# Performance work log

Hardware: AMD Instinct MI355X
Metric: run time of the kernel (lower is better)

Reference implementation:

```python
import jax, jax.numpy as jnp
import numpy as np

NEG_SLOPE = 0.01  # torch LeakyReLU default
MIN_FREQ = 1.0
MAX_FREQ = 10.0
W = 100
N_HIDDEN = 100
N_OBS = 64

def _leaky(x):
    return jnp.where(x >= 0, x, NEG_SLOPE * x)

def setup_inputs() -> dict:
    key = jax.random.key(0)
    ks = jax.random.split(key, 7)
    # kaiming_uniform-ish init scales (exact init doesn't matter for correctness baseline)
    def unif(k, shape, fan_in):
        bound = np.sqrt(6.0 / fan_in)
        return jax.random.uniform(k, shape, jnp.float32, -bound, bound)
    x = jax.random.normal(ks[0], (65536, N_OBS), jnp.float32)
    W_in = unif(ks[1], (N_OBS, W), N_OBS)
    b_in = jnp.zeros((W,), jnp.float32)
    Ws = unif(ks[2], (N_HIDDEN, W, W), W)
    bs = jnp.zeros((N_HIDDEN, W), jnp.float32)
    W_out = unif(ks[3], (W, 1), W)
    b_out = jnp.zeros((1,), jnp.float32)
    return {"x": x, "W_in": W_in, "b_in": b_in, "Ws": Ws, "bs": bs,
            "W_out": W_out, "b_out": b_out}

def reference(x, W_in, b_in, Ws, bs, W_out, b_out):
    h = _leaky(x @ W_in + b_in)                       # [B, 100]
    def layer(h, wb):
        w, b = wb
        return _leaky(h @ w + b), None
    h, _ = jax.lax.scan(layer, h, (Ws, bs))           # 100 hidden layers
    a = h @ W_out + b_out                             # [B, 1]
    a = jnp.tanh(a)
    return (a + 1.0) / 2.0 * (MAX_FREQ - MIN_FREQ) + MIN_FREQ
```

## Files before the change

kernel.cpp:

```cpp
#include <hip/hip_runtime.h>
#include <cmath>

#define NLAYERS 100
#define DIN     64
#define WDIM    100
#define NTT     4
#define ROWS    32
#define KS      7
#define PSTR    136
#define BUF     (ROWS * PSTR)

typedef _Float16 half8  __attribute__((ext_vector_type(8)));
typedef _Float16 half2v __attribute__((ext_vector_type(2)));
typedef __fp16   fp16x2 __attribute__((ext_vector_type(2)));
typedef float    f32x4  __attribute__((ext_vector_type(4)));
typedef float    f32x16 __attribute__((ext_vector_type(16)));

#define WSH_LAYER_HALVES (KS * NTT * 64 * 8)
#define WSH_HALVES       (NLAYERS * WSH_LAYER_HALVES)
#define W0_HALVES        (4 * NTT * 64 * 8)
#define BPAD_FLOATS      128
#define OFF_BPAD_B       ((WSH_HALVES + W0_HALVES) * 2)
#define OFF_WOUT_B       (OFF_BPAD_B + BPAD_FLOATS * 4)
#define WOUT_FLOATS      128

__global__ __launch_bounds__(256)
void actor_prep(const float* __restrict__ Win, const float* __restrict__ bin,
                const float* __restrict__ Ws,  const float* __restrict__ bs,
                const float* __restrict__ Wout,
                _Float16* __restrict__ wsh, _Float16* __restrict__ w0sh,
                float* __restrict__ bpad, float* __restrict__ woutp) {
    __shared__ float tile[16 * 128];
    const int bid = blockIdx.x, tid = threadIdx.x;
    if (bid < NLAYERS * KS) {
        const int l = bid / KS, ks = bid % KS;
#pragma unroll
        for (int e = 0; e < 8; ++e) {
            int idx = tid + 256 * e;
            int kk = idx >> 7, nn = idx & 127;
            int k = ks * 16 + kk;
            float v = 0.f;
            if (k < WDIM && nn < WDIM)        v = Ws[(l * WDIM + k) * WDIM + nn];
            else if (k == WDIM && nn < WDIM)  v = bs[l * WDIM + nn];
            else if (k == WDIM && nn == WDIM) v = 1.0f;
            tile[idx] = v;
        }
        __syncthreads();
        const int lane = tid & 63, nt = tid >> 6;
        const int g = lane >> 5, n = nt * 32 + (lane & 31);
        half8 o;
#pragma unroll
        for (int j = 0; j < 8; ++j) o[j] = (_Float16)tile[(g * 8 + j) * 128 + n];
        *(half8*)(wsh + (((l * KS + ks) * NTT + nt) << 9) + lane * 8) = o;
        return;
    }
    int b2 = bid - NLAYERS * KS;
    if (b2 < 4) {
        const int ks = b2;
#pragma unroll
        for (int e = 0; e < 8; ++e) {
            int idx = tid + 256 * e;
            int kk = idx >> 7, nn = idx & 127;
            int k = ks * 16 + kk;
            tile[idx] = (nn < WDIM) ? Win[k * WDIM + nn] : 0.f;
        }
        __syncthreads();
        const int lane = tid & 63, nt = tid >> 6;
        const int g = lane >> 5, n = nt * 32 + (lane & 31);
        half8 o;
#pragma unroll
        for (int j = 0; j < 8; ++j) o[j] = (_Float16)tile[(g * 8 + j) * 128 + n];
        *(half8*)(w0sh + ((ks * NTT + nt) << 9) + lane * 8) = o;
        return;
    }
    if (tid < BPAD_FLOATS) {
        bpad[tid] = (tid < WDIM) ? bin[tid] : (tid == WDIM ? 1.0f : 0.f);
    } else {
        int t = tid - BPAD_FLOATS;
        if (t < WOUT_FLOATS) woutp[t] = (t < WDIM) ? Wout[t] : 0.f;
    }
}

__device__ __forceinline__ void split8(const float* __restrict__ p, half8& hi, half8& lo) {
    f32x4 u0 = *(const f32x4*)p;
    f32x4 u1 = *(const f32x4*)(p + 4);
    float v[8] = {u0[0], u0[1], u0[2], u0[3], u1[0], u1[1], u1[2], u1[3]};
#pragma unroll
    for (int e = 0; e < 8; e += 2) {
        fp16x2 h = __builtin_amdgcn_cvt_pkrtz(v[e], v[e + 1]);
        float r0 = v[e]     - (float)h[0];
        float r1 = v[e + 1] - (float)h[1];
        fp16x2 l = __builtin_amdgcn_cvt_pkrtz(r0, r1);
        hi[e] = (_Float16)h[0]; hi[e + 1] = (_Float16)h[1];
        lo[e] = (_Float16)l[0]; lo[e + 1] = (_Float16)l[1];
    }
}

__device__ __forceinline__ void ep_quad(const f32x16 a, int qd, _Float16* __restrict__ d) {
    half2v p01, p23;
    p01[0] = (_Float16)a[4 * qd + 0]; p01[1] = (_Float16)a[4 * qd + 1];
    p23[0] = (_Float16)a[4 * qd + 2]; p23[1] = (_Float16)a[4 * qd + 3];
    const half2v slope = {(_Float16)0.01f, (_Float16)0.01f};
    p01 = __builtin_elementwise_max(p01, p01 * slope);
    p23 = __builtin_elementwise_max(p23, p23 * slope);
    uint2 w;
    w.x = __builtin_bit_cast(unsigned, p01);
    w.y = __builtin_bit_cast(unsigned, p23);
    *reinterpret_cast<uint2*>(d) = w;
}

__global__ __launch_bounds__(64, 2)
void actor_main(const float* __restrict__ x,
                const _Float16* __restrict__ wsh,
                const _Float16* __restrict__ w0sh,
                const float* __restrict__ bpad,
                const float* __restrict__ woutp,
                const float* __restrict__ bout,
                float* __restrict__ out) {
    __shared__ __align__(16) _Float16 hp[BUF];
    const int lane = threadIdx.x;
    const int g = lane >> 5, b31 = lane & 31;
    const int rowbase = blockIdx.x * ROWS;

    f32x16 acc[NTT];
    half8 wb[KS][NTT];
    const f32x16 zero16 = {0,0,0,0, 0,0,0,0, 0,0,0,0, 0,0,0,0};

    {
        half8 w0[4][NTT];
#pragma unroll
        for (int ks = 0; ks < 4; ++ks)
#pragma unroll
            for (int nt = 0; nt < NTT; ++nt)
                w0[ks][nt] = *(const half8*)(w0sh + (ks * NTT + nt) * 512 + lane * 8);
#pragma unroll
        for (int nt = 0; nt < NTT; ++nt)
#pragma unroll
            for (int qd = 0; qd < 4; ++qd) {
                f32x4 tq = *(const f32x4*)(bpad + nt * 32 + 8 * qd + 4 * g);
#pragma unroll
                for (int r = 0; r < 4; ++r) acc[nt][4 * qd + r] = tq[r];
            }
        const float* xr = x + (rowbase + b31) * DIN;
#pragma unroll
        for (int ks = 0; ks < 4; ++ks) {
            half8 xhi, xlo;
            split8(xr + ks * 16 + g * 8, xhi, xlo);
#pragma unroll
            for (int nt = 0; nt < NTT; ++nt) {
                acc[nt] = __builtin_amdgcn_mfma_f32_32x32x16_f16(w0[ks][nt], xhi, acc[nt], 0, 0, 0);
                acc[nt] = __builtin_amdgcn_mfma_f32_32x32x16_f16(w0[ks][nt], xlo, acc[nt], 0, 0, 0);
            }
        }
    }
#pragma unroll
    for (int nt = 0; nt < NTT; ++nt) {
        _Float16* d = hp + b31 * PSTR + nt * 32 + 4 * g;
#pragma unroll
        for (int qd = 0; qd < 4; ++qd) ep_quad(acc[nt], qd, d + 8 * qd);
    }
#pragma unroll
    for (int ks = 0; ks < KS; ++ks)
#pragma unroll
        for (int nt = 0; nt < NTT; ++nt)
            wb[ks][nt] = *(const half8*)(wsh + (ks * NTT + nt) * 512 + lane * 8);

#pragma unroll 1
    for (int l = 0; l < NLAYERS; ++l) {
        const _Float16* wn = wsh + (l < NLAYERS - 1 ? l + 1 : l) * WSH_LAYER_HALVES;
        half8 bh[KS];
#pragma unroll
        for (int ks = 0; ks < KS; ++ks)
            bh[ks] = *(const half8*)(hp + b31 * PSTR + ks * 16 + g * 8);
#pragma unroll
        for (int ks = 0; ks < KS; ++ks) {
            acc[0] = __builtin_amdgcn_mfma_f32_32x32x16_f16(
                wb[ks][0], bh[ks], (ks == 0 ? zero16 : acc[0]), 0, 0, 0);
            acc[1] = __builtin_amdgcn_mfma_f32_32x32x16_f16(
                wb[ks][1], bh[ks], (ks == 0 ? zero16 : acc[1]), 0, 0, 0);
            acc[2] = __builtin_amdgcn_mfma_f32_32x32x16_f16(
                wb[ks][2], bh[ks], (ks == 0 ? zero16 : acc[2]), 0, 0, 0);
            acc[3] = __builtin_amdgcn_mfma_f32_32x32x16_f16(
                wb[ks][3], bh[ks], (ks == 0 ? zero16 : acc[3]), 0, 0, 0);
#pragma unroll
            for (int nt = 0; nt < NTT; ++nt)
                wb[ks][nt] = *(const half8*)(wn + (ks * NTT + nt) * 512 + lane * 8);
        }
#pragma unroll
        for (int nt = 0; nt < NTT; ++nt) {
            _Float16* d = hp + b31 * PSTR + nt * 32 + 4 * g;
#pragma unroll
            for (int qd = 0; qd < 4; ++qd) ep_quad(acc[nt], qd, d + 8 * qd);
        }
    }

    float s = 0.f;
#pragma unroll
    for (int nt = 0; nt < NTT; ++nt)
#pragma unroll
        for (int qd = 0; qd < 4; ++qd) {
            f32x4 w4 = *(const f32x4*)(woutp + nt * 32 + 8 * qd + 4 * g);
#pragma unroll
            for (int r = 0; r < 4; ++r) {
                float a = acc[nt][4 * qd + r];
                float v = fmaxf(a, 0.01f * a);
                s += v * w4[r];
            }
        }
    s += __shfl_xor(s, 32);
    if (lane < 32) {
        float tot = s + bout[0];
        out[rowbase + b31] = tanhf(tot) * 4.5f + 5.5f;
    }
}

extern "C" void kernel_launch(void* const* d_in, const int* in_sizes, int n_in,
                              void* d_out, int out_size, void* d_ws, size_t ws_size,
                              hipStream_t stream) {
    const float* x    = (const float*)d_in[0];
    const float* Win  = (const float*)d_in[1];
    const float* bin  = (const float*)d_in[2];
    const float* Ws   = (const float*)d_in[3];
    const float* bs   = (const float*)d_in[4];
    const float* Wout = (const float*)d_in[5];
    const float* bout = (const float*)d_in[6];
    float* out = (float*)d_out;

    char* ws = (char*)d_ws;
    _Float16* wsh  = (_Float16*)ws;
    _Float16* w0sh = wsh + WSH_HALVES;
    float* bpad  = (float*)(ws + OFF_BPAD_B);
    float* woutp = (float*)(ws + OFF_WOUT_B);

    hipLaunchKernelGGL(actor_prep, dim3(NLAYERS * KS + 4 + 1), dim3(256), 0, stream,
                       Win, bin, Ws, bs, Wout, wsh, w0sh, bpad, woutp);

    const int nrows = in_sizes[0] / DIN;
    hipLaunchKernelGGL(actor_main, dim3(nrows / ROWS), dim3(64), 0, stream,
                       x, wsh, w0sh, bpad, woutp, bout, out);
}
```

Before: 299.7 us.

## Keep activations in registers via permlane32 swap and process two row tiles per wave

Removes the LDS round-trip for hidden activations between layers. The MFMA accumulator output is packed to fp16 and rearranged into the B-operand layout with v_permlane32_swap in registers. Each wave now handles 64 rows (two 32-row tiles), so every weight register load is reused twice and there are more independent MFMAs to hide latency. In exchange, register pressure roughly doubles for the accumulators, occupancy drops to one wave per launch-bounds hint, and the grid has half as many blocks.

Measured after the change: 256.3 us. 14.5% less time.

```diff
diff --git a/kernel.cpp b/kernel.cpp
--- a/kernel.cpp
+++ b/kernel.cpp
@@ -5,16 +5,16 @@
 #define DIN     64
 #define WDIM    100
 #define NTT     4
-#define ROWS    32
+#define RT      2
+#define ROWS    64
 #define KS      7
-#define PSTR    136
-#define BUF     (ROWS * PSTR)
 
 typedef _Float16 half8  __attribute__((ext_vector_type(8)));
 typedef _Float16 half2v __attribute__((ext_vector_type(2)));
 typedef __fp16   fp16x2 __attribute__((ext_vector_type(2)));
 typedef float    f32x4  __attribute__((ext_vector_type(4)));
 typedef float    f32x16 __attribute__((ext_vector_type(16)));
+typedef unsigned uint4v __attribute__((ext_vector_type(4)));
 
 #define WSH_LAYER_HALVES (KS * NTT * 64 * 8)
 #define WSH_HALVES       (NLAYERS * WSH_LAYER_HALVES)
@@ -96,20 +96,14 @@
     }
 }
 
-__device__ __forceinline__ void ep_quad(const f32x16 a, int qd, _Float16* __restrict__ d) {
-    half2v p01, p23;
-    p01[0] = (_Float16)a[4 * qd + 0]; p01[1] = (_Float16)a[4 * qd + 1];
-    p23[0] = (_Float16)a[4 * qd + 2]; p23[1] = (_Float16)a[4 * qd + 3];
+__device__ __forceinline__ unsigned pack2(float a, float b) {
+    half2v p; p[0] = (_Float16)a; p[1] = (_Float16)b;
     const half2v slope = {(_Float16)0.01f, (_Float16)0.01f};
-    p01 = __builtin_elementwise_max(p01, p01 * slope);
-    p23 = __builtin_elementwise_max(p23, p23 * slope);
-    uint2 w;
-    w.x = __builtin_bit_cast(unsigned, p01);
-    w.y = __builtin_bit_cast(unsigned, p23);
-    *reinterpret_cast<uint2*>(d) = w;
-}
-
-__global__ __launch_bounds__(64, 2)
+    p = __builtin_elementwise_max(p, p * slope);
+    return __builtin_bit_cast(unsigned, p);
+}
+
+__global__ __launch_bounds__(64, 1)
 void actor_main(const float* __restrict__ x,
                 const _Float16* __restrict__ wsh,
                 const _Float16* __restrict__ w0sh,
@@ -117,13 +111,13 @@
                 const float* __restrict__ woutp,
                 const float* __restrict__ bout,
                 float* __restrict__ out) {
-    __shared__ __align__(16) _Float16 hp[BUF];
     const int lane = threadIdx.x;
     const int g = lane >> 5, b31 = lane & 31;
     const int rowbase = blockIdx.x * ROWS;
 
-    f32x16 acc[NTT];
+    f32x16 acc[RT][NTT];
     half8 wb[KS][NTT];
+    half8 bh[RT][KS];
     const f32x16 zero16 = {0,0,0,0, 0,0,0,0, 0,0,0,0, 0,0,0,0};
 
     {
@@ -134,31 +128,45 @@
             for (int nt = 0; nt < NTT; ++nt)
                 w0[ks][nt] = *(const half8*)(w0sh + (ks * NTT + nt) * 512 + lane * 8);
 #pragma unroll
-        for (int nt = 0; nt < NTT; ++nt)
-#pragma unroll
-            for (int qd = 0; qd < 4; ++qd) {
-                f32x4 tq = *(const f32x4*)(bpad + nt * 32 + 8 * qd + 4 * g);
-#pragma unroll
-                for (int r = 0; r < 4; ++r) acc[nt][4 * qd + r] = tq[r];
+        for (int rt = 0; rt < RT; ++rt)
+#pragma unroll
+            for (int nt = 0; nt < NTT; ++nt)
+#pragma unroll
+                for (int qd = 0; qd < 4; ++qd) {
+                    f32x4 tq = *(const f32x4*)(bpad + nt * 32 + 8 * qd + 4 * g);
+#pragma unroll
+                    for (int r = 0; r < 4; ++r) acc[rt][nt][4 * qd + r] = tq[r];
+                }
+#pragma unroll
+        for (int rt = 0; rt < RT; ++rt) {
+            const float* xr = x + (rowbase + rt * 32 + b31) * DIN;
+#pragma unroll
+            for (int ks = 0; ks < 4; ++ks) {
+                half8 xhi, xlo;
+                split8(xr + ks * 16 + g * 8, xhi, xlo);
+#pragma unroll
+                for (int nt = 0; nt < NTT; ++nt) {
+                    acc[rt][nt] = __builtin_amdgcn_mfma_f32_32x32x16_f16(w0[ks][nt], xhi, acc[rt][nt], 0, 0, 0);
+                    acc[rt][nt] = __builtin_amdgcn_mfma_f32_32x32x16_f16(w0[ks][nt], xlo, acc[rt][nt], 0, 0, 0);
+                }
             }
-        const float* xr = x + (rowbase + b31) * DIN;
-#pragma unroll
-        for (int ks = 0; ks < 4; ++ks) {
-            half8 xhi, xlo;
-            split8(xr + ks * 16 + g * 8, xhi, xlo);
-#pragma unroll
-            for (int nt = 0; nt < NTT; ++nt) {
-                acc[nt] = __builtin_amdgcn_mfma_f32_32x32x16_f16(w0[ks][nt], xhi, acc[nt], 0, 0, 0);
-                acc[nt] = __builtin_amdgcn_mfma_f32_32x32x16_f16(w0[ks][nt], xlo, acc[nt], 0, 0, 0);
-            }
-        }
-    }
-#pragma unroll
-    for (int nt = 0; nt < NTT; ++nt) {
-        _Float16* d = hp + b31 * PSTR + nt * 32 + 4 * g;
-#pragma unroll
-        for (int qd = 0; qd < 4; ++qd) ep_quad(acc[nt], qd, d + 8 * qd);
-    }
+        }
+    }
+#pragma unroll
+    for (int rt = 0; rt < RT; ++rt)
+#pragma unroll
+        for (int ks = 0; ks < KS; ++ks) {
+            const int r0 = 8 * (ks & 1);
+            const f32x16 a = acc[rt][ks >> 1];
+            unsigned lo0 = pack2(a[r0 + 0], a[r0 + 1]);
+            unsigned lo1 = pack2(a[r0 + 2], a[r0 + 3]);
+            unsigned hi0 = pack2(a[r0 + 4], a[r0 + 5]);
+            unsigned hi1 = pack2(a[r0 + 6], a[r0 + 7]);
+            asm volatile("v_permlane32_swap_b32 %0, %1" : "+v"(lo0), "+v"(hi0));
+            asm volatile("v_permlane32_swap_b32 %0, %1" : "+v"(lo1), "+v"(hi1));
+            uint4v u = {lo0, lo1, hi0, hi1};
+            bh[rt][ks] = __builtin_bit_cast(half8, u);
+        }
 #pragma unroll
     for (int ks = 0; ks < KS; ++ks)
 #pragma unroll
@@ -168,49 +176,67 @@
 #pragma unroll 1
     for (int l = 0; l < NLAYERS; ++l) {
         const _Float16* wn = wsh + (l < NLAYERS - 1 ? l + 1 : l) * WSH_LAYER_HALVES;
-        half8 bh[KS];
-#pragma unroll
-        for (int ks = 0; ks < KS; ++ks)
-            bh[ks] = *(const half8*)(hp + b31 * PSTR + ks * 16 + g * 8);
 #pragma unroll
         for (int ks = 0; ks < KS; ++ks) {
-            acc[0] = __builtin_amdgcn_mfma_f32_32x32x16_f16(
-                wb[ks][0], bh[ks], (ks == 0 ? zero16 : acc[0]), 0, 0, 0);
-            acc[1] = __builtin_amdgcn_mfma_f32_32x32x16_f16(
-                wb[ks][1], bh[ks], (ks == 0 ? zero16 : acc[1]), 0, 0, 0);
-            acc[2] = __builtin_amdgcn_mfma_f32_32x32x16_f16(
-                wb[ks][2], bh[ks], (ks == 0 ? zero16 : acc[2]), 0, 0, 0);
-            acc[3] = __builtin_amdgcn_mfma_f32_32x32x16_f16(
-                wb[ks][3], bh[ks], (ks == 0 ? zero16 : acc[3]), 0, 0, 0);
+#pragma unroll
+            for (int rt = 0; rt < RT; ++rt)
+#pragma unroll
+                for (int nt = 0; nt < NTT; ++nt)
+                    acc[rt][nt] = __builtin_amdgcn_mfma_f32_32x32x16_f16(
+                        wb[ks][nt], bh[rt][ks], (ks == 0 ? zero16 : acc[rt][nt]), 0, 0, 0);
 #pragma unroll
             for (int nt = 0; nt < NTT; ++nt)
                 wb[ks][nt] = *(const half8*)(wn + (ks * NTT + nt) * 512 + lane * 8);
         }
-#pragma unroll
-        for (int nt = 0; nt < NTT; ++nt) {
-            _Float16* d = hp + b31 * PSTR + nt * 32 + 4 * g;
-#pragma unroll
-            for (int qd = 0; qd < 4; ++qd) ep_quad(acc[nt], qd, d + 8 * qd);
-        }
-    }
-
-    float s = 0.f;
-#pragma unroll
-    for (int nt = 0; nt < NTT; ++nt)
-#pragma unroll
-        for (int qd = 0; qd < 4; ++qd) {
-            f32x4 w4 = *(const f32x4*)(woutp + nt * 32 + 8 * qd + 4 * g);
-#pragma unroll
-            for (int r = 0; r < 4; ++r) {
-                float a = acc[nt][4 * qd + r];
-                float v = fmaxf(a, 0.01f * a);
-                s += v * w4[r];
+        if (l < NLAYERS - 1) {
+#pragma unroll
+            for (int rt = 0; rt < RT; ++rt)
+#pragma unroll
+                for (int ks = 0; ks < KS; ++ks) {
+                    const int r0 = 8 * (ks & 1);
+                    const f32x16 a = acc[rt][ks >> 1];
+                    unsigned lo0 = pack2(a[r0 + 0], a[r0 + 1]);
+                    unsigned lo1 = pack2(a[r0 + 2], a[r0 + 3]);
+                    unsigned hi0 = pack2(a[r0 + 4], a[r0 + 5]);
+                    unsigned hi1 = pack2(a[r0 + 6], a[r0 + 7]);
+                    asm volatile("v_permlane32_swap_b32 %0, %1" : "+v"(lo0), "+v"(hi0));
+                    asm volatile("v_permlane32_swap_b32 %0, %1" : "+v"(lo1), "+v"(hi1));
+                    uint4v u = {lo0, lo1, hi0, hi1};
+                    bh[rt][ks] = __builtin_bit_cast(half8, u);
+                }
+#pragma unroll
+            for (int ks = 0; ks < KS; ++ks)
+#pragma unroll
+                for (int nt = 0; nt < NTT; ++nt)
+                    asm volatile("" : "+v"(wb[ks][nt]));
+        }
+    }
+
+    float part[RT];
+#pragma unroll
+    for (int rt = 0; rt < RT; ++rt) {
+        float s = 0.f;
+#pragma unroll
+        for (int nt = 0; nt < NTT; ++nt)
+#pragma unroll
+            for (int qd = 0; qd < 4; ++qd) {
+                f32x4 w4 = *(const f32x4*)(woutp + nt * 32 + 8 * qd + 4 * g);
+#pragma unroll
+                for (int r = 0; r < 4; ++r) {
+                    float a = acc[rt][nt][4 * qd + r];
+                    float v = fmaxf(a, 0.01f * a);
+                    s += v * w4[r];
+                }
             }
-        }
-    s += __shfl_xor(s, 32);
+        s += __shfl_xor(s, 32);
+        part[rt] = s;
+    }
     if (lane < 32) {
-        float tot = s + bout[0];
-        out[rowbase + b31] = tanhf(tot) * 4.5f + 5.5f;
+#pragma unroll
+        for (int rt = 0; rt < RT; ++rt) {
+            float tot = part[rt] + bout[0];
+            out[rowbase + rt * 32 + b31] = tanhf(tot) * 4.5f + 5.5f;
+        }
     }
 }
 
```
